# Kernel tuning notes

Measured on AMD Instinct MI355X. Metric: run time of the kernel, lower is better.

## Reference

```python
import jax, jax.numpy as jnp
import numpy as np

B, S, D = 4, 1024, 1024
H, DH = 16, 64
F = 4 * D
EPS = 1e-6


def _ln(x, scale, bias, axes=-1):
    mean = jnp.mean(x, axis=axes, keepdims=True)
    var = jnp.var(x, axis=axes, keepdims=True)
    return (x - mean) * jax.lax.rsqrt(var + EPS) * scale + bias


def setup_inputs() -> dict:
    key = jax.random.key(0)
    ks = jax.random.split(key, 20)
    sd = 1.0 / np.sqrt(D)
    sf = 1.0 / np.sqrt(F)
    inp = {
        'x': jax.random.normal(ks[0], (B, S, D), jnp.float32),
        'z': jax.random.normal(ks[1], (B, S, D), jnp.float32),
        'ln1_s': jnp.ones((D,), jnp.float32),
        'ln1_b': jnp.zeros((D,), jnp.float32),
        'Wq': jax.random.normal(ks[2], (D, D), jnp.float32) * sd,
        'bq': jnp.zeros((D,), jnp.float32),
        'Wk': jax.random.normal(ks[3], (D, D), jnp.float32) * sd,
        'bk': jnp.zeros((D,), jnp.float32),
        'Wv': jax.random.normal(ks[4], (D, D), jnp.float32) * sd,
        'bv': jnp.zeros((D,), jnp.float32),
        'qn_s': jnp.ones((H, DH), jnp.float32),
        'qn_b': jnp.zeros((H, DH), jnp.float32),
        'kn_s': jnp.ones((H, DH), jnp.float32),
        'kn_b': jnp.zeros((H, DH), jnp.float32),
        'Wo': jax.random.normal(ks[5], (D, D), jnp.float32) * sd,
        'bo': jnp.zeros((D,), jnp.float32),
        'ln2_s': jnp.ones((D,), jnp.float32),
        'ln2_b': jnp.zeros((D,), jnp.float32),
        'W1': jax.random.normal(ks[6], (D, F), jnp.float32) * sd,
        'b1': jnp.zeros((F,), jnp.float32),
        'W2': jax.random.normal(ks[7], (D, F), jnp.float32) * sd,
        'b2': jnp.zeros((F,), jnp.float32),
        'W3': jax.random.normal(ks[8], (F, D), jnp.float32) * sf,
        'b3': jnp.zeros((D,), jnp.float32),
    }
    return inp


def reference(x, z, ln1_s, ln1_b, Wq, bq, Wk, bk, Wv, bv, qn_s, qn_b, kn_s, kn_b,
              Wo, bo, ln2_s, ln2_b, W1, b1, W2, b2, W3, b3):
    # z is unused by the original module body
    x_skip = x
    xn = _ln(x, ln1_s, ln1_b)
    q = (xn @ Wq + bq).reshape(B, S, H, DH)
    k = (xn @ Wk + bk).reshape(B, S, H, DH)
    v = (xn @ Wv + bv).reshape(B, S, H, DH)
    # QK-norm: flax LayerNorm(feature_axes=(-2,-1)) still reduces over axis -1,
    # but carries (H, DH)-shaped scale/bias
    q = _ln(q, qn_s, qn_b)
    k = _ln(k, kn_s, kn_b)
    attn = jnp.einsum('bqhd,bkhd->bhqk', q, k) / jnp.sqrt(jnp.asarray(DH, q.dtype))
    attn = jax.nn.softmax(attn, axis=-1)
    out = jnp.einsum('bhqk,bkhd->bqhd', attn, v).reshape(B, S, D)
    x = x_skip + out @ Wo + bo
    x_skip = x
    xn = _ln(x, ln2_s, ln2_b)
    x1 = xn @ W1 + b1
    x2 = xn @ W2 + b2
    h = x1 * jax.nn.gelu(x2, approximate=True)  # GeGLU
    x = x_skip + h @ W3 + b3
    return x
```

## Files before the change

kernel.cpp:

```cpp
#include <hip/hip_runtime.h>

typedef unsigned short u16;
typedef __bf16  bfrag  __attribute__((ext_vector_type(8)));
typedef float   f32x4  __attribute__((ext_vector_type(4)));
typedef u16     u16x8  __attribute__((ext_vector_type(8)));
typedef u16     u16x4  __attribute__((ext_vector_type(4)));

__device__ __forceinline__ float bf2f(u16 u) {
    unsigned v = ((unsigned)u) << 16;
    return __builtin_bit_cast(float, v);
}
__device__ __forceinline__ u16 f2bf(float f) {
    unsigned x = __builtin_bit_cast(unsigned, f);
    unsigned r = (x + 0x7fffu + ((x >> 16) & 1u)) >> 16;
    return (u16)r;
}
__device__ __forceinline__ void g2l16(const u16* g, u16* l) {
    __builtin_amdgcn_global_load_lds((__attribute__((address_space(1))) void*)g,
                                     (__attribute__((address_space(3))) void*)l, 16, 0, 0);
}
__device__ __forceinline__ float gelu_tanh(float x) {
    float c = 1.5957691216057308f * (x + 0.044715f * x * x * x);
    return x * __frcp_rn(1.0f + __expf(-c));
}

#define SW64(l)   (((((l) & 7) ^ (((l) >> 3) & 7))) * 8)
#define RS64(kk, quad, l15)  (((((kk) * 4 + (quad)) ^ ((l15) & 7))) * 8)

__global__ __launch_bounds__(256) void wtln(
        const float* __restrict__ Wq, const float* __restrict__ Wk,
        const float* __restrict__ Wv, const float* __restrict__ Wo,
        const float* __restrict__ W1, const float* __restrict__ W2,
        const float* __restrict__ W3,
        u16* __restrict__ WqkvT, u16* __restrict__ WoT,
        u16* __restrict__ W12T, u16* __restrict__ W3T,
        const float* __restrict__ x, const float* __restrict__ ln1_s,
        const float* __restrict__ ln1_b, u16* __restrict__ xn1) {
    __shared__ float tile[64][65];
    int blk = blockIdx.x;
    if (blk >= 4096) {
        int row = blk - 4096, t = threadIdx.x;
        float4 v = ((const float4*)(x + (size_t)row * 1024))[t];
        float sum = v.x + v.y + v.z + v.w;
        float sq  = v.x * v.x + v.y * v.y + v.z * v.z + v.w * v.w;
#pragma unroll
        for (int off = 1; off < 64; off <<= 1) {
            sum += __shfl_xor(sum, off);
            sq  += __shfl_xor(sq,  off);
        }
        float* s1 = &tile[0][0];
        float* s2 = &tile[0][8];
        int wave = t >> 6;
        if ((t & 63) == 0) { s1[wave] = sum; s2[wave] = sq; }
        __syncthreads();
        sum = s1[0] + s1[1] + s1[2] + s1[3];
        sq  = s2[0] + s2[1] + s2[2] + s2[3];
        float mean = sum * (1.0f / 1024.0f);
        float var  = sq  * (1.0f / 1024.0f) - mean * mean;
        float inv  = rsqrtf(var + 1e-6f);
        float4 sc = ((const float4*)ln1_s)[t], bb = ((const float4*)ln1_b)[t];
        u16x4 o;
        o[0] = f2bf((v.x - mean) * inv * sc.x + bb.x);
        o[1] = f2bf((v.y - mean) * inv * sc.y + bb.y);
        o[2] = f2bf((v.z - mean) * inv * sc.z + bb.z);
        o[3] = f2bf((v.w - mean) * inv * sc.w + bb.w);
        *(u16x4*)&xn1[(size_t)row * 1024 + t * 4] = o;
        return;
    }
    const float* W; u16* Wt; int R, C, local;
    if (blk < 768) {
        int w = blk >> 8; local = blk & 255;
        W = (w == 0) ? Wq : (w == 1) ? Wk : Wv;
        Wt = WqkvT + (size_t)w * 1024 * 1024; R = 1024; C = 1024;
    } else if (blk < 1024) { W = Wo; Wt = WoT; R = 1024; C = 1024; local = blk - 768; }
    else if (blk < 2048)   { W = W1; Wt = W12T; R = 1024; C = 4096; local = blk - 1024; }
    else if (blk < 3072)   { W = W2; Wt = W12T + (size_t)4096 * 1024; R = 1024; C = 4096; local = blk - 2048; }
    else                   { W = W3; Wt = W3T; R = 4096; C = 1024; local = blk - 3072; }
    int tiles_x = C >> 6;
    int c0 = (local % tiles_x) * 64, r0 = (local / tiles_x) * 64;
    int t = threadIdx.x;
    int lr = t >> 4, lc = (t & 15) * 4;
#pragma unroll
    for (int p = 0; p < 4; p++) {
        float4 v = *(const float4*)&W[(size_t)(r0 + p * 16 + lr) * C + c0 + lc];
        *(float4*)&tile[p * 16 + lr][lc] = v;
    }
    __syncthreads();
    int oc = t >> 2;
    int rs = (t & 3) * 16;
    u16x8 o0, o1;
#pragma unroll
    for (int j = 0; j < 8; j++) o0[j] = f2bf(tile[rs + j][oc]);
#pragma unroll
    for (int j = 0; j < 8; j++) o1[j] = f2bf(tile[rs + 8 + j][oc]);
    u16* dst = &Wt[(size_t)(c0 + oc) * R + r0 + rs];
    *(u16x8*)dst       = o0;
    *(u16x8*)(dst + 8) = o1;
}

template <int EPI>
__global__ __launch_bounds__(256, 3) void gemm64(const u16* __restrict__ A,
                                                 const u16* __restrict__ Bt,
                                                 const float* __restrict__ bias,
                                                 const float* __restrict__ bias2,
                                                 const float* __restrict__ bias3,
                                                 const float* __restrict__ qn_s,
                                                 const float* __restrict__ qn_b,
                                                 const float* __restrict__ kn_s,
                                                 const float* __restrict__ kn_b,
                                                 u16* __restrict__ o0,
                                                 u16* __restrict__ o1,
                                                 u16* __restrict__ o2,
                                                 u16* __restrict__ o3,
                                                 int M, int N, int K, int Klen) {
    __shared__ u16 As[128 * 64];
    __shared__ u16 Bs[128 * 64];
    int tid = threadIdx.x, wave = tid >> 6, lane = tid & 63;
    int quad = lane >> 4, l15 = lane & 15;
    int row0 = blockIdx.y * 128, col0 = blockIdx.x * 128;
    int kz = blockIdx.z;
    int klen = (kz == (int)gridDim.z - 1) ? K - kz * Klen : Klen;
    int wr = (wave >> 1) * 64, wc = (wave & 1) * 64;
    int swz = SW64(lane);

    f32x4 acc[4][4] = {};

    const u16* gA = A  + (size_t)(row0 + wave * 32 + (lane >> 3)) * K + kz * Klen + swz;
    const u16* gB = Bt + (size_t)(col0 + wave * 32 + (lane >> 3)) * K + kz * Klen + swz;
    u16* lA = &As[wave * 32 * 64];
    u16* lB = &Bs[wave * 32 * 64];

    for (int k0 = 0; k0 < klen; k0 += 64) {
        __syncthreads();
#pragma unroll
        for (int j = 0; j < 4; j++) {
            g2l16(gA + k0 + j * 8 * K, lA + j * 8 * 64);
            g2l16(gB + k0 + j * 8 * K, lB + j * 8 * 64);
        }
        __syncthreads();
#pragma unroll
        for (int kk = 0; kk < 2; kk++) {
            int rs = RS64(kk, quad, l15);
            bfrag af[4], bf[4];
#pragma unroll
            for (int mi = 0; mi < 4; mi++)
                af[mi] = *(const bfrag*)&As[(wr + mi * 16 + l15) * 64 + rs];
#pragma unroll
            for (int ni = 0; ni < 4; ni++)
                bf[ni] = *(const bfrag*)&Bs[(wc + ni * 16 + l15) * 64 + rs];
#pragma unroll
            for (int mi = 0; mi < 4; mi++)
#pragma unroll
                for (int ni = 0; ni < 4; ni++)
                    acc[mi][ni] = __builtin_amdgcn_mfma_f32_16x16x32_bf16(
                        af[mi], bf[ni], acc[mi][ni], 0, 0, 0);
        }
    }

    if (EPI == 0) {
        u16* P = (kz == 0) ? o0 : (kz == 1) ? o1 : (kz == 2) ? o2 : o3;
#pragma unroll
        for (int mi = 0; mi < 4; mi++) {
            int rbase = row0 + wr + mi * 16 + quad * 4;
#pragma unroll
            for (int r = 0; r < 4; r++)
#pragma unroll
                for (int ni = 0; ni < 4; ni++)
                    P[(size_t)(rbase + r) * N + col0 + wc + ni * 16 + l15] =
                        f2bf(acc[mi][ni][r]);
        }
    } else {
        int cbase = col0 + wc;
        int z = cbase >> 10;
        int hd = (cbase >> 6) & 15;
        const float* bp = (z == 0) ? bias : (z == 1) ? bias2 : bias3;
        float post = (z == 0) ? 0.125f : 1.0f;
        float bv[4], sn[4], bn[4];
#pragma unroll
        for (int ni = 0; ni < 4; ni++)
            bv[ni] = bp[(cbase & 1023) + ni * 16 + l15];
        if (z < 2) {
            const float* ns = (z == 0) ? qn_s : kn_s;
            const float* nb = (z == 0) ? qn_b : kn_b;
#pragma unroll
            for (int ni = 0; ni < 4; ni++) {
                sn[ni] = ns[hd * 64 + ni * 16 + l15];
                bn[ni] = nb[hd * 64 + ni * 16 + l15];
            }
        }
#pragma unroll
        for (int mi = 0; mi < 4; mi++) {
            int rbase = row0 + wr + mi * 16 + quad * 4;
#pragma unroll
            for (int r = 0; r < 4; r++) {
                float v0 = acc[mi][0][r] + bv[0];
                float v1 = acc[mi][1][r] + bv[1];
                float v2 = acc[mi][2][r] + bv[2];
                float v3 = acc[mi][3][r] + bv[3];
                size_t rb = (size_t)(rbase + r) * N + cbase;
                if (z == 2) {
                    o0[rb + 0 * 16 + l15] = f2bf(v0);
                    o0[rb + 1 * 16 + l15] = f2bf(v1);
                    o0[rb + 2 * 16 + l15] = f2bf(v2);
                    o0[rb + 3 * 16 + l15] = f2bf(v3);
                } else {
                    float s  = v0 + v1 + v2 + v3;
                    float sq = v0 * v0 + v1 * v1 + v2 * v2 + v3 * v3;
#pragma unroll
                    for (int m = 1; m < 16; m <<= 1) {
                        s  += __shfl_xor(s,  m);
                        sq += __shfl_xor(sq, m);
                    }
                    float mean = s * (1.0f / 64.0f);
                    float var  = sq * (1.0f / 64.0f) - mean * mean;
                    float inv  = rsqrtf(var + 1e-6f);
                    o0[rb + 0 * 16 + l15] = f2bf(((v0 - mean) * inv * sn[0] + bn[0]) * post);
                    o0[rb + 1 * 16 + l15] = f2bf(((v1 - mean) * inv * sn[1] + bn[1]) * post);
                    o0[rb + 2 * 16 + l15] = f2bf(((v2 - mean) * inv * sn[2] + bn[2]) * post);
                    o0[rb + 3 * 16 + l15] = f2bf(((v3 - mean) * inv * sn[3] + bn[3]) * post);
                }
            }
        }
    }
}

__global__ __launch_bounds__(256, 2) void gemm_w12(const u16* __restrict__ A,
                                                   const u16* __restrict__ W12T,
                                                   const float* __restrict__ b1,
                                                   const float* __restrict__ b2,
                                                   u16* __restrict__ H) {
    __shared__ u16 As[128 * 64];
    __shared__ u16 B1s[128 * 64];
    __shared__ u16 B2s[128 * 64];
    int tid = threadIdx.x, wave = tid >> 6, lane = tid & 63;
    int quad = lane >> 4, l15 = lane & 15;
    int row0 = blockIdx.y * 128, col0 = blockIdx.x * 128;
    int wr = (wave >> 1) * 64, wc = (wave & 1) * 64;
    int swz = SW64(lane);

    f32x4 acc1[4][4] = {}, acc2[4][4] = {};

    const u16* gA  = A    + (size_t)(row0 + wave * 32 + (lane >> 3)) * 1024 + swz;
    const u16* gB1 = W12T + (size_t)(col0 + wave * 32 + (lane >> 3)) * 1024 + swz;
    const u16* gB2 = gB1  + (size_t)4096 * 1024;
    u16* lA  = &As [wave * 32 * 64];
    u16* lB1 = &B1s[wave * 32 * 64];
    u16* lB2 = &B2s[wave * 32 * 64];

    for (int k0 = 0; k0 < 1024; k0 += 64) {
        __syncthreads();
#pragma unroll
        for (int j = 0; j < 4; j++) {
            g2l16(gA  + k0 + j * 8 * 1024, lA  + j * 8 * 64);
            g2l16(gB1 + k0 + j * 8 * 1024, lB1 + j * 8 * 64);
            g2l16(gB2 + k0 + j * 8 * 1024, lB2 + j * 8 * 64);
        }
        __syncthreads();
#pragma unroll
        for (int kk = 0; kk < 2; kk++) {
            int rs = RS64(kk, quad, l15);
            bfrag af[4], b1f[4], b2f[4];
#pragma unroll
            for (int mi = 0; mi < 4; mi++)
                af[mi] = *(const bfrag*)&As[(wr + mi * 16 + l15) * 64 + rs];
#pragma unroll
            for (int ni = 0; ni < 4; ni++) {
                b1f[ni] = *(const bfrag*)&B1s[(wc + ni * 16 + l15) * 64 + rs];
                b2f[ni] = *(const bfrag*)&B2s[(wc + ni * 16 + l15) * 64 + rs];
            }
#pragma unroll
            for (int mi = 0; mi < 4; mi++)
#pragma unroll
                for (int ni = 0; ni < 4; ni++) {
                    acc1[mi][ni] = __builtin_amdgcn_mfma_f32_16x16x32_bf16(
                        af[mi], b1f[ni], acc1[mi][ni], 0, 0, 0);
                    acc2[mi][ni] = __builtin_amdgcn_mfma_f32_16x16x32_bf16(
                        af[mi], b2f[ni], acc2[mi][ni], 0, 0, 0);
                }
        }
    }

    float bv1[4], bv2[4];
    int cols[4];
#pragma unroll
    for (int ni = 0; ni < 4; ni++) {
        cols[ni] = col0 + wc + ni * 16 + l15;
        bv1[ni] = b1[cols[ni]];
        bv2[ni] = b2[cols[ni]];
    }
#pragma unroll
    for (int mi = 0; mi < 4; mi++) {
        int rbase = row0 + wr + mi * 16 + quad * 4;
#pragma unroll
        for (int r = 0; r < 4; r++) {
#pragma unroll
            for (int ni = 0; ni < 4; ni++) {
                float x1 = acc1[mi][ni][r] + bv1[ni];
                float x2 = acc2[mi][ni][r] + bv2[ni];
                H[(size_t)(rbase + r) * 4096 + cols[ni]] = f2bf(x1 * gelu_tanh(x2));
            }
        }
    }
}

__global__ __launch_bounds__(256) void reduce_ln(const u16* __restrict__ p0,
                                                 const u16* __restrict__ p1,
                                                 const float* __restrict__ x,
                                                 const float* __restrict__ bo,
                                                 const float* __restrict__ s,
                                                 const float* __restrict__ b,
                                                 float* __restrict__ xmid,
                                                 u16* __restrict__ xn2) {
    int row = blockIdx.x, t = threadIdx.x;
    size_t i = (size_t)row * 1024 + t * 4;
    float4 xv = *(const float4*)&x[i];
    float4 bb = *(const float4*)&bo[t * 4];
    u16x4 a0 = *(const u16x4*)&p0[i];
    u16x4 a1 = *(const u16x4*)&p1[i];
    float4 v;
    v.x = xv.x + bb.x + bf2f(a0[0]) + bf2f(a1[0]);
    v.y = xv.y + bb.y + bf2f(a0[1]) + bf2f(a1[1]);
    v.z = xv.z + bb.z + bf2f(a0[2]) + bf2f(a1[2]);
    v.w = xv.w + bb.w + bf2f(a0[3]) + bf2f(a1[3]);
    *(float4*)&xmid[i] = v;
    float sum = v.x + v.y + v.z + v.w;
    float sq  = v.x * v.x + v.y * v.y + v.z * v.z + v.w * v.w;
#pragma unroll
    for (int off = 1; off < 64; off <<= 1) {
        sum += __shfl_xor(sum, off);
        sq  += __shfl_xor(sq,  off);
    }
    __shared__ float s1[4], s2[4];
    int wave = t >> 6;
    if ((t & 63) == 0) { s1[wave] = sum; s2[wave] = sq; }
    __syncthreads();
    sum = s1[0] + s1[1] + s1[2] + s1[3];
    sq  = s2[0] + s2[1] + s2[2] + s2[3];
    float mean = sum * (1.0f / 1024.0f);
    float var  = sq  * (1.0f / 1024.0f) - mean * mean;
    float inv  = rsqrtf(var + 1e-6f);
    float4 sc = ((const float4*)s)[t], lb = ((const float4*)b)[t];
    u16x4 o;
    o[0] = f2bf((v.x - mean) * inv * sc.x + lb.x);
    o[1] = f2bf((v.y - mean) * inv * sc.y + lb.y);
    o[2] = f2bf((v.z - mean) * inv * sc.z + lb.z);
    o[3] = f2bf((v.w - mean) * inv * sc.w + lb.w);
    *(u16x4*)&xn2[i] = o;
}

__global__ __launch_bounds__(256) void reduce3(const u16* __restrict__ p0,
                                               const u16* __restrict__ p1,
                                               const u16* __restrict__ p2,
                                               const float* __restrict__ xmid,
                                               const float* __restrict__ b3,
                                               float* __restrict__ out) {
    size_t i = ((size_t)blockIdx.x * 256 + threadIdx.x) * 4;
    float4 xm = *(const float4*)&xmid[i];
    float4 bb = *(const float4*)&b3[i & 1023];
    u16x4 a0 = *(const u16x4*)&p0[i];
    u16x4 a1 = *(const u16x4*)&p1[i];
    u16x4 a2 = *(const u16x4*)&p2[i];
    float4 o;
    o.x = xm.x + bb.x + bf2f(a0[0]) + bf2f(a1[0]) + bf2f(a2[0]);
    o.y = xm.y + bb.y + bf2f(a0[1]) + bf2f(a1[1]) + bf2f(a2[1]);
    o.z = xm.z + bb.z + bf2f(a0[2]) + bf2f(a1[2]) + bf2f(a2[2]);
    o.w = xm.w + bb.w + bf2f(a0[3]) + bf2f(a1[3]) + bf2f(a2[3]);
    *(float4*)&out[i] = o;
}

#define LPK 72
#define LPV 72
#define LPP 68
__global__ __launch_bounds__(256, 2) void flash(const u16* __restrict__ qkv,
                                                u16* __restrict__ o) {
    int qt = blockIdx.x, h = blockIdx.y, b = blockIdx.z;
    int tid = threadIdx.x, wave = tid >> 6, lane = tid & 63;
    int quad = lane >> 4, l15 = lane & 15;

    __shared__ u16 Ks[64 * LPK];
    __shared__ u16 Vt[64 * LPV];
    __shared__ u16 Ps[128 * LPP];

    bfrag aq[2][2];
#pragma unroll
    for (int g = 0; g < 2; g++) {
        const u16* qrow = qkv
            + (size_t)(b * 1024 + qt * 128 + g * 64 + wave * 16 + l15) * 3072
            + h * 64 + quad * 8;
        aq[g][0] = *(const bfrag*)qrow;
        aq[g][1] = *(const bfrag*)(qrow + 32);
    }

    int krow = tid >> 2, kseg = tid & 3;
    const u16* kbase = qkv + (size_t)(b * 1024 + krow) * 3072 + 1024
                       + h * 64 + kseg * 16;
    const u16* vbase = qkv + (size_t)(b * 1024 + lane) * 3072 + 2048
                       + h * 64 + wave * 16;

    u16x8 k0 = *(const u16x8*)kbase;
    u16x8 k1 = *(const u16x8*)(kbase + 8);
    u16x8 v0 = *(const u16x8*)vbase;
    u16x8 v1 = *(const u16x8*)(vbase + 8);

    f32x4 accO[2][4] = {};
    float l_run[2][4] = {};

    for (int kt = 0; kt < 16; kt++) {
        __syncthreads();
        *(u16x8*)&Ks[krow * LPK + kseg * 16]     = k0;
        *(u16x8*)&Ks[krow * LPK + kseg * 16 + 8] = k1;
#pragma unroll
        for (int j = 0; j < 8; j++) Vt[(wave * 16 + j) * LPV + lane]     = v0[j];
#pragma unroll
        for (int j = 0; j < 8; j++) Vt[(wave * 16 + 8 + j) * LPV + lane] = v1[j];
        if (kt < 15) {
            const u16* kn = kbase + (size_t)(kt + 1) * 64 * 3072;
            const u16* vn = vbase + (size_t)(kt + 1) * 64 * 3072;
            k0 = *(const u16x8*)kn;
            k1 = *(const u16x8*)(kn + 8);
            v0 = *(const u16x8*)vn;
            v1 = *(const u16x8*)(vn + 8);
        }
        __syncthreads();

        bfrag bkf[4][2];
#pragma unroll
        for (int ct = 0; ct < 4; ct++) {
            bkf[ct][0] = *(const bfrag*)&Ks[(ct * 16 + l15) * LPK + quad * 8];
            bkf[ct][1] = *(const bfrag*)&Ks[(ct * 16 + l15) * LPK + 32 + quad * 8];
        }

#pragma unroll
        for (int g = 0; g < 2; g++) {
            f32x4 accS[4] = {};
#pragma unroll
            for (int ct = 0; ct < 4; ct++) {
                accS[ct] = __builtin_amdgcn_mfma_f32_16x16x32_bf16(
                    aq[g][0], bkf[ct][0], accS[ct], 0, 0, 0);
                accS[ct] = __builtin_amdgcn_mfma_f32_16x16x32_bf16(
                    aq[g][1], bkf[ct][1], accS[ct], 0, 0, 0);
            }

#pragma unroll
            for (int r = 0; r < 4; r++) {
                float p0 = __expf(accS[0][r]);
                float p1 = __expf(accS[1][r]);
                float p2 = __expf(accS[2][r]);
                float p3 = __expf(accS[3][r]);
                l_run[g][r] += (p0 + p1) + (p2 + p3);
                int pbase = (g * 64 + wave * 16 + quad * 4 + r) * LPP + l15;
                Ps[pbase + 0]  = f2bf(p0);
                Ps[pbase + 16] = f2bf(p1);
                Ps[pbase + 32] = f2bf(p2);
                Ps[pbase + 48] = f2bf(p3);
            }

#pragma unroll
            for (int kk = 0; kk < 2; kk++) {
                const u16* pp = &Ps[(g * 64 + wave * 16 + l15) * LPP
                                    + kk * 32 + quad * 8];
                u16x4 lo = *(const u16x4*)pp;
                u16x4 hi = *(const u16x4*)(pp + 4);
                u16x8 apu;
                apu[0] = lo[0]; apu[1] = lo[1]; apu[2] = lo[2]; apu[3] = lo[3];
                apu[4] = hi[0]; apu[5] = hi[1]; apu[6] = hi[2]; apu[7] = hi[3];
                bfrag ap = __builtin_bit_cast(bfrag, apu);
#pragma unroll
                for (int oc = 0; oc < 4; oc++) {
                    bfrag bv = *(const bfrag*)&Vt[(oc * 16 + l15) * LPV
                                                  + kk * 32 + quad * 8];
                    accO[g][oc] = __builtin_amdgcn_mfma_f32_16x16x32_bf16(
                        ap, bv, accO[g][oc], 0, 0, 0);
                }
            }
        }
    }

#pragma unroll
    for (int g = 0; g < 2; g++)
#pragma unroll
    for (int r = 0; r < 4; r++) {
        float l = l_run[g][r];
#pragma unroll
        for (int m = 1; m < 16; m <<= 1) l += __shfl_xor(l, m);
        float linv = 1.0f / l;
        int srow = qt * 128 + g * 64 + wave * 16 + quad * 4 + r;
#pragma unroll
        for (int oc = 0; oc < 4; oc++)
            o[(size_t)(b * 1024 + srow) * 1024 + h * 64 + oc * 16 + l15] =
                f2bf(accO[g][oc][r] * linv);
    }
}

extern "C" void kernel_launch(void* const* d_in, const int* in_sizes, int n_in,
                              void* d_out, int out_size, void* d_ws, size_t ws_size,
                              hipStream_t stream) {
    const float* x     = (const float*)d_in[0];
    const float* ln1_s = (const float*)d_in[2];
    const float* ln1_b = (const float*)d_in[3];
    const float* Wq = (const float*)d_in[4];  const float* bq = (const float*)d_in[5];
    const float* Wk = (const float*)d_in[6];  const float* bk = (const float*)d_in[7];
    const float* Wv = (const float*)d_in[8];  const float* bv = (const float*)d_in[9];
    const float* qn_s = (const float*)d_in[10]; const float* qn_b = (const float*)d_in[11];
    const float* kn_s = (const float*)d_in[12]; const float* kn_b = (const float*)d_in[13];
    const float* Wo = (const float*)d_in[14]; const float* bo = (const float*)d_in[15];
    const float* ln2_s = (const float*)d_in[16]; const float* ln2_b = (const float*)d_in[17];
    const float* W1 = (const float*)d_in[18]; const float* b1 = (const float*)d_in[19];
    const float* W2 = (const float*)d_in[20]; const float* b2 = (const float*)d_in[21];
    const float* W3 = (const float*)d_in[22]; const float* b3 = (const float*)d_in[23];
    float* out = (float*)d_out;

    char* ws = (char*)d_ws;
    const size_t MB = (size_t)1 << 20;
    u16* WqkvT = (u16*)(ws + 0);
    u16* WoT   = (u16*)(ws + 6 * MB);
    u16* W12T  = (u16*)(ws + 8 * MB);
    u16* W3T   = (u16*)(ws + 24 * MB);
    u16* xn1   = (u16*)(ws + 32 * MB);
    u16* attn  = (u16*)(ws + 32 * MB);
    u16* xn2   = (u16*)(ws + 32 * MB);
    u16* qkv   = (u16*)(ws + 40 * MB);
    float* xmid = (float*)(ws + 40 * MB);
    u16* h     = (u16*)(ws + 64 * MB);
    u16* wp0   = (u16*)(ws + 64 * MB);
    u16* wp1   = (u16*)(ws + 72 * MB);
    u16* p0    = (u16*)(ws + 0);
    u16* p1    = (u16*)(ws + 8 * MB);
    u16* p2    = (u16*)(ws + 16 * MB);

    wtln<<<8192, 256, 0, stream>>>(Wq, Wk, Wv, Wo, W1, W2, W3,
                                   WqkvT, WoT, W12T, W3T,
                                   x, ln1_s, ln1_b, xn1);

    gemm64<4><<<dim3(24, 32, 1), 256, 0, stream>>>(
        xn1, WqkvT, bq, bk, bv, qn_s, qn_b, kn_s, kn_b,
        qkv, nullptr, nullptr, nullptr, 4096, 3072, 1024, 1024);

    flash<<<dim3(8, 16, 4), 256, 0, stream>>>(qkv, attn);

    gemm64<0><<<dim3(8, 32, 2), 256, 0, stream>>>(
        attn, WoT, nullptr, nullptr, nullptr, nullptr, nullptr, nullptr, nullptr,
        wp0, wp1, nullptr, nullptr, 4096, 1024, 1024, 512);

    reduce_ln<<<4096, 256, 0, stream>>>(wp0, wp1, x, bo, ln2_s, ln2_b, xmid, xn2);

    gemm_w12<<<dim3(32, 32), 256, 0, stream>>>(xn2, W12T, b1, b2, h);

    gemm64<0><<<dim3(8, 32, 3), 256, 0, stream>>>(
        h, W3T, nullptr, nullptr, nullptr, nullptr, nullptr, nullptr, nullptr,
        p0, p1, p2, nullptr, 4096, 1024, 4096, 1344);

    reduce3<<<4096, 256, 0, stream>>>(p0, p1, p2, xmid, b3, out);
}
```

Before: 380.6 us.

## Process two K/V tiles per barrier in flash and split Wo GEMM three ways

The flash attention loop now stages two 64-row K/V tiles per iteration in doubled LDS buffers, with a two-tile register prefetch. This halves the number of __syncthreads barriers and store/load phases. Separately, the Wo projection GEMM uses three split-K partitions instead of two, giving more blocks to fill the CUs, and reduce_ln now sums a third partial buffer. The cost is more LDS and registers in flash, which may hurt occupancy, and an extra partial buffer write and read in the reduction.

```diff
diff --git a/kernel.cpp b/kernel.cpp
--- a/kernel.cpp
+++ b/kernel.cpp
@@ -305,6 +305,7 @@
 
 __global__ __launch_bounds__(256) void reduce_ln(const u16* __restrict__ p0,
                                                  const u16* __restrict__ p1,
+                                                 const u16* __restrict__ p2,
                                                  const float* __restrict__ x,
                                                  const float* __restrict__ bo,
                                                  const float* __restrict__ s,
@@ -317,11 +318,12 @@
     float4 bb = *(const float4*)&bo[t * 4];
     u16x4 a0 = *(const u16x4*)&p0[i];
     u16x4 a1 = *(const u16x4*)&p1[i];
+    u16x4 a2 = *(const u16x4*)&p2[i];
     float4 v;
-    v.x = xv.x + bb.x + bf2f(a0[0]) + bf2f(a1[0]);
-    v.y = xv.y + bb.y + bf2f(a0[1]) + bf2f(a1[1]);
-    v.z = xv.z + bb.z + bf2f(a0[2]) + bf2f(a1[2]);
-    v.w = xv.w + bb.w + bf2f(a0[3]) + bf2f(a1[3]);
+    v.x = xv.x + bb.x + bf2f(a0[0]) + bf2f(a1[0]) + bf2f(a2[0]);
+    v.y = xv.y + bb.y + bf2f(a0[1]) + bf2f(a1[1]) + bf2f(a2[1]);
+    v.z = xv.z + bb.z + bf2f(a0[2]) + bf2f(a1[2]) + bf2f(a2[2]);
+    v.w = xv.w + bb.w + bf2f(a0[3]) + bf2f(a1[3]) + bf2f(a2[3]);
     *(float4*)&xmid[i] = v;
     float sum = v.x + v.y + v.z + v.w;
     float sq  = v.x * v.x + v.y * v.y + v.z * v.z + v.w * v.w;
@@ -377,8 +379,8 @@
     int tid = threadIdx.x, wave = tid >> 6, lane = tid & 63;
     int quad = lane >> 4, l15 = lane & 15;
 
-    __shared__ u16 Ks[64 * LPK];
-    __shared__ u16 Vt[64 * LPV];
+    __shared__ u16 Ks[2][64 * LPK];
+    __shared__ u16 Vt[2][64 * LPV];
     __shared__ u16 Ps[128 * LPP];
 
     bfrag aq[2][2];
@@ -397,80 +399,97 @@
     const u16* vbase = qkv + (size_t)(b * 1024 + lane) * 3072 + 2048
                        + h * 64 + wave * 16;
 
-    u16x8 k0 = *(const u16x8*)kbase;
-    u16x8 k1 = *(const u16x8*)(kbase + 8);
-    u16x8 v0 = *(const u16x8*)vbase;
-    u16x8 v1 = *(const u16x8*)(vbase + 8);
+    u16x8 kr[2][2], vr[2][2];
+#pragma unroll
+    for (int s = 0; s < 2; s++) {
+        const u16* kn = kbase + (size_t)s * 64 * 3072;
+        const u16* vn = vbase + (size_t)s * 64 * 3072;
+        kr[s][0] = *(const u16x8*)kn;
+        kr[s][1] = *(const u16x8*)(kn + 8);
+        vr[s][0] = *(const u16x8*)vn;
+        vr[s][1] = *(const u16x8*)(vn + 8);
+    }
 
     f32x4 accO[2][4] = {};
     float l_run[2][4] = {};
 
-    for (int kt = 0; kt < 16; kt++) {
-        __syncthreads();
-        *(u16x8*)&Ks[krow * LPK + kseg * 16]     = k0;
-        *(u16x8*)&Ks[krow * LPK + kseg * 16 + 8] = k1;
-#pragma unroll
-        for (int j = 0; j < 8; j++) Vt[(wave * 16 + j) * LPV + lane]     = v0[j];
-#pragma unroll
-        for (int j = 0; j < 8; j++) Vt[(wave * 16 + 8 + j) * LPV + lane] = v1[j];
-        if (kt < 15) {
-            const u16* kn = kbase + (size_t)(kt + 1) * 64 * 3072;
-            const u16* vn = vbase + (size_t)(kt + 1) * 64 * 3072;
-            k0 = *(const u16x8*)kn;
-            k1 = *(const u16x8*)(kn + 8);
-            v0 = *(const u16x8*)vn;
-            v1 = *(const u16x8*)(vn + 8);
-        }
-        __syncthreads();
-
-        bfrag bkf[4][2];
-#pragma unroll
-        for (int ct = 0; ct < 4; ct++) {
-            bkf[ct][0] = *(const bfrag*)&Ks[(ct * 16 + l15) * LPK + quad * 8];
-            bkf[ct][1] = *(const bfrag*)&Ks[(ct * 16 + l15) * LPK + 32 + quad * 8];
-        }
-
-#pragma unroll
-        for (int g = 0; g < 2; g++) {
-            f32x4 accS[4] = {};
+    for (int kt = 0; kt < 16; kt += 2) {
+        __syncthreads();
+#pragma unroll
+        for (int s = 0; s < 2; s++) {
+            *(u16x8*)&Ks[s][krow * LPK + kseg * 16]     = kr[s][0];
+            *(u16x8*)&Ks[s][krow * LPK + kseg * 16 + 8] = kr[s][1];
+#pragma unroll
+            for (int j = 0; j < 8; j++)
+                Vt[s][(wave * 16 + j) * LPV + lane]     = vr[s][0][j];
+#pragma unroll
+            for (int j = 0; j < 8; j++)
+                Vt[s][(wave * 16 + 8 + j) * LPV + lane] = vr[s][1][j];
+        }
+        if (kt < 14) {
+#pragma unroll
+            for (int s = 0; s < 2; s++) {
+                const u16* kn = kbase + (size_t)(kt + 2 + s) * 64 * 3072;
+                const u16* vn = vbase + (size_t)(kt + 2 + s) * 64 * 3072;
+                kr[s][0] = *(const u16x8*)kn;
+                kr[s][1] = *(const u16x8*)(kn + 8);
+                vr[s][0] = *(const u16x8*)vn;
+                vr[s][1] = *(const u16x8*)(vn + 8);
+            }
+        }
+        __syncthreads();
+
+#pragma unroll
+        for (int s = 0; s < 2; s++) {
+            bfrag bkf[4][2];
 #pragma unroll
             for (int ct = 0; ct < 4; ct++) {
-                accS[ct] = __builtin_amdgcn_mfma_f32_16x16x32_bf16(
-                    aq[g][0], bkf[ct][0], accS[ct], 0, 0, 0);
-                accS[ct] = __builtin_amdgcn_mfma_f32_16x16x32_bf16(
-                    aq[g][1], bkf[ct][1], accS[ct], 0, 0, 0);
-            }
-
-#pragma unroll
-            for (int r = 0; r < 4; r++) {
-                float p0 = __expf(accS[0][r]);
-                float p1 = __expf(accS[1][r]);
-                float p2 = __expf(accS[2][r]);
-                float p3 = __expf(accS[3][r]);
-                l_run[g][r] += (p0 + p1) + (p2 + p3);
-                int pbase = (g * 64 + wave * 16 + quad * 4 + r) * LPP + l15;
-                Ps[pbase + 0]  = f2bf(p0);
-                Ps[pbase + 16] = f2bf(p1);
-                Ps[pbase + 32] = f2bf(p2);
-                Ps[pbase + 48] = f2bf(p3);
-            }
-
-#pragma unroll
-            for (int kk = 0; kk < 2; kk++) {
-                const u16* pp = &Ps[(g * 64 + wave * 16 + l15) * LPP
-                                    + kk * 32 + quad * 8];
-                u16x4 lo = *(const u16x4*)pp;
-                u16x4 hi = *(const u16x4*)(pp + 4);
-                u16x8 apu;
-                apu[0] = lo[0]; apu[1] = lo[1]; apu[2] = lo[2]; apu[3] = lo[3];
-                apu[4] = hi[0]; apu[5] = hi[1]; apu[6] = hi[2]; apu[7] = hi[3];
-                bfrag ap = __builtin_bit_cast(bfrag, apu);
-#pragma unroll
-                for (int oc = 0; oc < 4; oc++) {
-                    bfrag bv = *(const bfrag*)&Vt[(oc * 16 + l15) * LPV
-                                                  + kk * 32 + quad * 8];
-                    accO[g][oc] = __builtin_amdgcn_mfma_f32_16x16x32_bf16(
-                        ap, bv, accO[g][oc], 0, 0, 0);
+                bkf[ct][0] = *(const bfrag*)&Ks[s][(ct * 16 + l15) * LPK + quad * 8];
+                bkf[ct][1] = *(const bfrag*)&Ks[s][(ct * 16 + l15) * LPK + 32 + quad * 8];
+            }
+
+#pragma unroll
+            for (int g = 0; g < 2; g++) {
+                f32x4 accS[4] = {};
+#pragma unroll
+                for (int ct = 0; ct < 4; ct++) {
+                    accS[ct] = __builtin_amdgcn_mfma_f32_16x16x32_bf16(
+                        aq[g][0], bkf[ct][0], accS[ct], 0, 0, 0);
+                    accS[ct] = __builtin_amdgcn_mfma_f32_16x16x32_bf16(
+                        aq[g][1], bkf[ct][1], accS[ct], 0, 0, 0);
+                }
+
+#pragma unroll
+                for (int r = 0; r < 4; r++) {
+                    float p0 = __expf(accS[0][r]);
+                    float p1 = __expf(accS[1][r]);
+                    float p2 = __expf(accS[2][r]);
+                    float p3 = __expf(accS[3][r]);
+                    l_run[g][r] += (p0 + p1) + (p2 + p3);
+                    int pbase = (g * 64 + wave * 16 + quad * 4 + r) * LPP + l15;
+                    Ps[pbase + 0]  = f2bf(p0);
+                    Ps[pbase + 16] = f2bf(p1);
+                    Ps[pbase + 32] = f2bf(p2);
+                    Ps[pbase + 48] = f2bf(p3);
+                }
+
+#pragma unroll
+                for (int kk = 0; kk < 2; kk++) {
+                    const u16* pp = &Ps[(g * 64 + wave * 16 + l15) * LPP
+                                        + kk * 32 + quad * 8];
+                    u16x4 lo = *(const u16x4*)pp;
+                    u16x4 hi = *(const u16x4*)(pp + 4);
+                    u16x8 apu;
+                    apu[0] = lo[0]; apu[1] = lo[1]; apu[2] = lo[2]; apu[3] = lo[3];
+                    apu[4] = hi[0]; apu[5] = hi[1]; apu[6] = hi[2]; apu[7] = hi[3];
+                    bfrag ap = __builtin_bit_cast(bfrag, apu);
+#pragma unroll
+                    for (int oc = 0; oc < 4; oc++) {
+                        bfrag bv = *(const bfrag*)&Vt[s][(oc * 16 + l15) * LPV
+                                                        + kk * 32 + quad * 8];
+                        accO[g][oc] = __builtin_amdgcn_mfma_f32_16x16x32_bf16(
+                            ap, bv, accO[g][oc], 0, 0, 0);
+                    }
                 }
             }
         }
@@ -524,6 +543,7 @@
     u16* h     = (u16*)(ws + 64 * MB);
     u16* wp0   = (u16*)(ws + 64 * MB);
     u16* wp1   = (u16*)(ws + 72 * MB);
+    u16* wp2   = (u16*)(ws + 80 * MB);
     u16* p0    = (u16*)(ws + 0);
     u16* p1    = (u16*)(ws + 8 * MB);
     u16* p2    = (u16*)(ws + 16 * MB);
@@ -538,11 +558,12 @@
 
     flash<<<dim3(8, 16, 4), 256, 0, stream>>>(qkv, attn);
 
-    gemm64<0><<<dim3(8, 32, 2), 256, 0, stream>>>(
+    gemm64<0><<<dim3(8, 32, 3), 256, 0, stream>>>(
         attn, WoT, nullptr, nullptr, nullptr, nullptr, nullptr, nullptr, nullptr,
-        wp0, wp1, nullptr, nullptr, 4096, 1024, 1024, 512);
-
-    reduce_ln<<<4096, 256, 0, stream>>>(wp0, wp1, x, bo, ln2_s, ln2_b, xmid, xn2);
+        wp0, wp1, wp2, nullptr, 4096, 1024, 1024, 320);
+
+    reduce_ln<<<4096, 256, 0, stream>>>(wp0, wp1, wp2, x, bo, ln2_s, ln2_b,
+                                        xmid, xn2);
 
     gemm_w12<<<dim3(32, 32), 256, 0, stream>>>(xn2, W12T, b1, b2, h);
 
```

Measured after the change: 395.2 us. 3.8% more time.
